# Optimization experiments

Hardware: AMD Instinct MI355X
Metric: run time of the kernel (lower is better)

## Reference

```python
import jax, jax.numpy as jnp
import numpy as np

B, H0, W0, C, NH, WS, SHIFT = 32, 48, 48, 384, 12, 12, 6
N = WS * WS
TAB = 2 * WS - 1  # 23


def _window_partition(x, ws):
    b, h, w, c = x.shape
    x = x.reshape(b, h // ws, ws, w // ws, ws, c)
    return x.transpose(0, 1, 3, 2, 4, 5).reshape(-1, ws, ws, c)


def _window_reverse(win, ws, h, w):
    b = win.shape[0] // (h * w // ws // ws)
    x = win.reshape(b, h // ws, w // ws, ws, ws, -1)
    return x.transpose(0, 1, 3, 2, 4, 5).reshape(b, h, w, -1)


def _ln(y, g, b):
    m = y.mean(-1, keepdims=True)
    v = y.var(-1, keepdims=True)
    return (y - m) * jax.lax.rsqrt(v + 1e-5) * g + b


def setup_inputs() -> dict:
    key = jax.random.key(0)
    ks = jax.random.split(key, 12)
    s = 0.02
    # relative coords table, normalized to [-1, 1]
    rng = np.arange(-(WS - 1), WS, dtype=np.float32) / (WS - 1)
    table = np.stack(np.meshgrid(rng, rng, indexing='ij'), axis=-1)[None]  # (1,23,23,2)
    # relative position index
    ch, cw = np.meshgrid(np.arange(WS), np.arange(WS), indexing='ij')
    coords = np.stack([ch, cw]).reshape(2, -1)
    rel = coords[:, :, None] - coords[:, None, :] + (WS - 1)
    rpi = (rel[0] * TAB + rel[1]).astype(np.int32)  # (N,N)
    # shifted-window attention mask
    img = np.zeros((1, H0, W0, 1), dtype=np.float32)
    cnt = 0
    sl = (slice(0, -WS), slice(-WS, -SHIFT), slice(-SHIFT, None))
    for hs in sl:
        for ws_ in sl:
            img[:, hs, ws_, :] = cnt
            cnt += 1
    mw = img.reshape(1, H0 // WS, WS, W0 // WS, WS, 1).transpose(0, 1, 3, 2, 4, 5).reshape(-1, N)
    diff = mw[:, None, :] - mw[:, :, None]
    attn_mask = np.where(diff != 0, -100.0, 0.0).astype(np.float32)  # (nW,N,N)
    Ch = C * 4
    return {
        'x': jax.random.normal(ks[0], (B, H0 * W0, C), jnp.float32),
        'relative_coords_table': jnp.asarray(table),
        'relative_position_index': jnp.asarray(rpi),
        'attn_mask': jnp.asarray(attn_mask),
        'qkv_w': jax.random.normal(ks[1], (C, 3 * C), jnp.float32) * s,
        'q_bias': jnp.zeros((C,), jnp.float32),
        'v_bias': jnp.zeros((C,), jnp.float32),
        'logit_scale': jnp.log(10.0 * jnp.ones((NH, 1, 1), jnp.float32)),
        'cpb_w1': jax.random.normal(ks[2], (2, 512), jnp.float32) * s,
        'cpb_b1': jnp.zeros((512,), jnp.float32),
        'cpb_w2': jax.random.normal(ks[3], (512, NH), jnp.float32) * s,
        'proj_w': jax.random.normal(ks[4], (C, C), jnp.float32) * s,
        'proj_b': jnp.zeros((C,), jnp.float32),
        'norm1_g': jnp.ones((C,), jnp.float32),
        'norm1_b': jnp.zeros((C,), jnp.float32),
        'norm2_g': jnp.ones((C,), jnp.float32),
        'norm2_b': jnp.zeros((C,), jnp.float32),
        'fc1_w': jax.random.normal(ks[5], (C, Ch), jnp.float32) * s,
        'fc1_b': jnp.zeros((Ch,), jnp.float32),
        'fc2_w': jax.random.normal(ks[6], (Ch, C), jnp.float32) * s,
        'fc2_b': jnp.zeros((C,), jnp.float32),
        'H': H0,
        'W': W0,
    }


def reference(x, relative_coords_table, relative_position_index, attn_mask,
              qkv_w, q_bias, v_bias, logit_scale, cpb_w1, cpb_b1, cpb_w2,
              proj_w, proj_b, norm1_g, norm1_b, norm2_g, norm2_b,
              fc1_w, fc1_b, fc2_w, fc2_b, H, W):
    b, L, c = x.shape
    hd = c // NH
    shortcut = x
    x4 = x.reshape(b, H, W, c)
    shifted = jnp.roll(x4, (-SHIFT, -SHIFT), axis=(1, 2))
    xw = _window_partition(shifted, WS).reshape(-1, N, c)  # (B_, N, C)
    qkv_bias = jnp.concatenate([q_bias, jnp.zeros_like(q_bias), v_bias])
    qkv = xw @ qkv_w + qkv_bias
    qkv = qkv.reshape(-1, N, 3, NH, hd).transpose(2, 0, 3, 1, 4)  # (3,B_,h,N,d)
    q, k, v = qkv[0], qkv[1], qkv[2]
    qn = q / jnp.maximum(jnp.linalg.norm(q, axis=-1, keepdims=True), 1e-12)
    kn = k / jnp.maximum(jnp.linalg.norm(k, axis=-1, keepdims=True), 1e-12)
    attn = jnp.einsum('bhnd,bhmd->bhnm', qn, kn)
    scale = jnp.exp(jnp.minimum(logit_scale, jnp.log(100.0)))  # clamp max=log(1/0.01)
    attn = attn * scale
    tab = jax.nn.relu(relative_coords_table @ cpb_w1 + cpb_b1) @ cpb_w2  # (1,23,23,h)
    tab = tab.reshape(-1, NH)
    bias = tab[relative_position_index.reshape(-1)].reshape(N, N, NH).transpose(2, 0, 1)
    bias = 16.0 * jax.nn.sigmoid(bias)
    attn = attn + bias[None]
    nW = attn_mask.shape[0]
    attn = attn.reshape(b, nW, NH, N, N) + attn_mask[None, :, None]
    attn = jax.nn.softmax(attn.reshape(-1, NH, N, N), axis=-1)
    out = jnp.einsum('bhnm,bhmd->bhnd', attn, v).transpose(0, 2, 1, 3).reshape(-1, N, c)
    out = out @ proj_w + proj_b
    out = _window_reverse(out.reshape(-1, WS, WS, c), WS, H, W)
    x4 = jnp.roll(out, (SHIFT, SHIFT), axis=(1, 2)).reshape(b, H * W, c)
    x = shortcut + _ln(x4, norm1_g, norm1_b)
    h = jax.nn.gelu(x @ fc1_w + fc1_b, approximate=False) @ fc2_w + fc2_b
    x = x + _ln(h, norm2_g, norm2_b)
    return x
```

## Files before the change

kernel.cpp:

```cpp
#include <hip/hip_runtime.h>


typedef unsigned int uint32;
typedef unsigned short u16;
typedef __attribute__((ext_vector_type(4))) float f32x4;
typedef __attribute__((ext_vector_type(8))) __bf16 bf16x8;

static __device__ __forceinline__ u16 f2bf(float f) {
    union { float f; uint32 u; } v; v.f = f;
    uint32 r = v.u + 0x7fffu + ((v.u >> 16) & 1u);
    return (u16)(r >> 16);
}
static __device__ __forceinline__ float bf2f(u16 h) {
    union { uint32 u; float f; } v; v.u = ((uint32)h) << 16; return v.f;
}
static __device__ __forceinline__ uint32 pack2(float a, float b) {
    return (uint32)f2bf(a) | ((uint32)f2bf(b) << 16);
}
static __device__ __forceinline__ float blo(uint32 u){ union{uint32 u;float f;}v; v.u=u<<16; return v.f; }
static __device__ __forceinline__ float bhi(uint32 u){ union{uint32 u;float f;}v; v.u=u&0xffff0000u; return v.f; }

typedef __attribute__((address_space(1))) const void gas_void;
typedef __attribute__((address_space(3))) void las_void;
static __device__ __forceinline__ void glds16(const void* g, void* l) {
    __builtin_amdgcn_global_load_lds((gas_void*)g, (las_void*)l, 16, 0, 0);
}

#define SWZ(c, row) ((c) ^ ((((row) >> 1) & 3) << 3))

#define VMCNT(N) asm volatile("s_waitcnt vmcnt(" #N ")" ::: "memory")
#define BARM() do { asm volatile("" ::: "memory"); __builtin_amdgcn_s_barrier(); asm volatile("" ::: "memory"); } while (0)

static __device__ __forceinline__ float fast_gelu(float x) {
    float z = x * 0.70710678118654752f;
    float az = fabsf(z);
    float t = __builtin_amdgcn_rcpf(fmaf(0.3275911f, az, 1.0f));
    float p = t * (0.254829592f + t * (-0.284496736f + t * (1.421413741f
              + t * (-1.453152027f + t * 1.061405429f))));
    float e = __expf(-z * z);
    float er = copysignf(fmaf(-p, e, 1.0f), z);
    return 0.5f * x * (1.0f + er);
}


__global__ void wt_convert(const float* __restrict__ W, u16* __restrict__ WT, int K, int N) {
    long idx = (long)blockIdx.x * 256 + threadIdx.x;
    long tot = (long)K * N;
    if (idx >= tot) return;
    int n = (int)(idx / K), k = (int)(idx - (long)n * K);
    WT[(long)n * K + SWZ(k, n)] = f2bf(W[(long)k * N + n]);
}

__global__ void build_qkv_bias(const float* __restrict__ qb, const float* __restrict__ vb,
                               float* __restrict__ outb) {
    int c = blockIdx.x * 256 + threadIdx.x;
    if (c >= 1152) return;
    outb[c] = (c < 384) ? qb[c] : ((c < 768) ? 0.f : vb[c - 768]);
}

__global__ void cpb_tab(const float* __restrict__ table, const float* __restrict__ w1,
                        const float* __restrict__ b1, const float* __restrict__ w2,
                        float* __restrict__ tab) {
    __shared__ float hid[512];
    int e = blockIdx.x;
    float tx = table[e * 2 + 0], ty = table[e * 2 + 1];
    for (int u = threadIdx.x; u < 512; u += 256)
        hid[u] = fmaxf(tx * w1[u] + ty * w1[512 + u] + b1[u], 0.f);
    __syncthreads();
    if (threadIdx.x < 12) {
        float s = 0.f;
        for (int u = 0; u < 512; ++u) s += hid[u] * w2[u * 12 + threadIdx.x];
        tab[e * 12 + threadIdx.x] = s;
    }
}

__global__ void cpb_bias(const float* __restrict__ tab, const int* __restrict__ rpi,
                         float* __restrict__ bias16) {
    int idx = blockIdx.x * 256 + threadIdx.x;
    if (idx >= 12 * 144 * 144) return;
    int h = idx / 20736, ij = idx - h * 20736;
    float t = tab[rpi[ij] * 12 + h];
    bias16[idx] = 16.f / (1.f + __expf(-t));
}

__global__ void gather_xbf(const float* __restrict__ x, u16* __restrict__ xw) {
    int idx = blockIdx.x * 256 + threadIdx.x;
    if (idx >= 73728 * 48) return;
    int row = idx / 48, c = (idx - row * 48) * 8;
    int win = row / 144, n = row - win * 144;
    int b = win >> 4, wi = win & 15;
    int r = n / 12, cc = n - r * 12;
    int sh = ((wi >> 2) * 12 + r + 6) % 48;
    int sw = ((wi & 3) * 12 + cc + 6) % 48;
    long src = ((long)(b * 2304 + sh * 48 + sw)) * 384 + c;
    float4 f0 = *(const float4*)(x + src);
    float4 f1 = *(const float4*)(x + src + 4);
    uint4 o;
    o.x = pack2(f0.x, f0.y); o.y = pack2(f0.z, f0.w);
    o.z = pack2(f1.x, f1.y); o.w = pack2(f1.z, f1.w);
    *(uint4*)(xw + (long)row * 384 + SWZ(c, row)) = o;
}


enum { EPI_QKV = 0, EPI_PLAIN = 1, EPI_GELU = 2 };

template<int EPI, bool OSWZ>
__global__ __launch_bounds__(256) void gemm_k(
    const u16* __restrict__ Ag, const u16* __restrict__ Bg,
    const float* __restrict__ bias, u16* __restrict__ outp,
    int N, int K, int ntn)
{
    __shared__ __align__(16) u16 As[3][128 * 32];
    __shared__ __align__(16) u16 Bs[3][128 * 32];
    const int tid = threadIdx.x, lane = tid & 63, wid = tid >> 6;
    const int qq = gridDim.x >> 3;
    const int wg = (blockIdx.x & 7) * qq + (blockIdx.x >> 3);
    const int mIdx = wg / ntn, nIdx = wg - mIdx * ntn;
    const int m0 = mIdx << 7, n0 = nIdx << 7;

    const int wrow = (wid >> 1) << 6, wcol = (wid & 1) << 6;
    const int fr = lane & 15, gsel = lane >> 4;

    const int s_r = (wid << 5) + (lane >> 2);
    const int s_g = (lane & 3) << 3;
    const long a_base = (long)(m0 + s_r) * K + s_g;
    const long b_base = (long)(n0 + s_r) * K + s_g;
    const long qstep = (long)16 * K;

    auto stage = [&](int buf, int kt) {
        const int k0 = kt << 5;
#pragma unroll
        for (int q = 0; q < 2; ++q) {
            glds16(Ag + a_base + qstep * q + k0, &As[buf][(wid * 32 + q * 16) * 32]);
            glds16(Bg + b_base + qstep * q + k0, &Bs[buf][(wid * 32 + q * 16) * 32]);
        }
    };

    int arow[4], acol[4], brow[4], bcol[4];
#pragma unroll
    for (int i = 0; i < 4; ++i) {
        arow[i] = wrow + i * 16 + fr; acol[i] = SWZ(gsel * 8, arow[i]);
        brow[i] = wcol + i * 16 + fr; bcol[i] = SWZ(gsel * 8, brow[i]);
    }

    f32x4 acc[4][4];
    const f32x4 zero4 = {0.f, 0.f, 0.f, 0.f};
#pragma unroll
    for (int i = 0; i < 4; ++i)
#pragma unroll
        for (int j = 0; j < 4; ++j) acc[i][j] = zero4;

    auto compute = [&](int buf) {
        bf16x8 af[4], bg[4];
#pragma unroll
        for (int i = 0; i < 4; ++i) af[i] = *(const bf16x8*)&As[buf][arow[i] * 32 + acol[i]];
#pragma unroll
        for (int j = 0; j < 4; ++j) bg[j] = *(const bf16x8*)&Bs[buf][brow[j] * 32 + bcol[j]];
#pragma unroll
        for (int i = 0; i < 4; ++i)
#pragma unroll
            for (int j = 0; j < 4; ++j)
                acc[i][j] = __builtin_amdgcn_mfma_f32_16x16x32_bf16(af[i], bg[j], acc[i][j], 0, 0, 0);
    };

    const int nk = K >> 5;
    stage(0, 0);
    stage(1, 1);
    int cur = 0, nxt = 2;
    for (int kt = 0; kt < nk - 1; ++kt) {
        VMCNT(4);
        BARM();
        if (kt + 2 < nk) { stage(nxt, kt + 2); nxt = (nxt == 2) ? 0 : nxt + 1; }
        compute(cur);
        cur = (cur == 2) ? 0 : cur + 1;
    }
    VMCNT(0);
    BARM();
    compute(cur);

    const int rbase = gsel << 2;
    if constexpr (EPI == EPI_QKV) {
        long coloff[4];
        float bv[4];
#pragma unroll
        for (int j = 0; j < 4; ++j) {
            int gn0 = n0 + wcol + j * 16;
            int which = gn0 / 384;
            int c = gn0 - which * 384;
            coloff[j] = (long)(which * 12 + (c >> 5)) * 4608 + (c & 31);
            bv[j] = bias[gn0 + fr];
        }
#pragma unroll
        for (int i = 0; i < 4; ++i) {
            long rowoff[4];
#pragma unroll
            for (int r = 0; r < 4; ++r) {
                int gm = m0 + wrow + i * 16 + rbase + r;
                int win = gm / 144, n = gm - win * 144;
                rowoff[r] = (long)win * 165888 + n * 32;
            }
#pragma unroll
            for (int j = 0; j < 4; ++j)
#pragma unroll
                for (int r = 0; r < 4; ++r)
                    outp[rowoff[r] + coloff[j] + fr] = f2bf(acc[i][j][r] + bv[j]);
        }
    } else {
        float bv[4];
#pragma unroll
        for (int j = 0; j < 4; ++j) bv[j] = bias[n0 + wcol + j * 16 + fr];
#pragma unroll
        for (int i = 0; i < 4; ++i) {
#pragma unroll
            for (int r = 0; r < 4; ++r) {
                const int gm = m0 + wrow + i * 16 + rbase + r;
                u16* orow = outp + (long)gm * N;
                const int sx = OSWZ ? (((gm >> 1) & 3) << 3) : 0;
#pragma unroll
                for (int j = 0; j < 4; ++j) {
                    const int gn = n0 + wcol + j * 16 + fr;
                    float v = acc[i][j][r] + bv[j];
                    if constexpr (EPI == EPI_GELU) v = fast_gelu(v);
                    orow[gn ^ sx] = f2bf(v);
                }
            }
        }
    }
}


__global__ __launch_bounds__(192) void attn_k(
    const u16* __restrict__ qkv,
    const float* __restrict__ bias16,
    const float* __restrict__ mask,
    const float* __restrict__ lsc,
    u16* __restrict__ attn_o)
{
    __shared__ __align__(16) u16 KL[144][40];
    __shared__ __align__(16) u16 VT[32][168];
    __shared__ __align__(16) u16 PL[3][16][168];
    const int blk = blockIdx.x;
    const int win = blk / 12, head = blk - win * 12;
    const int tid = threadIdx.x, lane = tid & 63, wid = tid >> 6;
    const long base = ((long)win * 36 + head) * 4608;
    const u16* Qp = qkv + base;
    const u16* Kp = qkv + base + 12 * 4608;
    const u16* Vp = qkv + base + 24 * 4608;
    const float scale = __expf(fminf(lsc[head], 4.6051701859880914f));

    if (tid < 144) {
        const uint4* s = (const uint4*)(Kp + tid * 32);
        uint4 uu[4] = { s[0], s[1], s[2], s[3] };
        float f[32];
#pragma unroll
        for (int q = 0; q < 4; ++q) {
            f[q*8+0]=blo(uu[q].x); f[q*8+1]=bhi(uu[q].x);
            f[q*8+2]=blo(uu[q].y); f[q*8+3]=bhi(uu[q].y);
            f[q*8+4]=blo(uu[q].z); f[q*8+5]=bhi(uu[q].z);
            f[q*8+6]=blo(uu[q].w); f[q*8+7]=bhi(uu[q].w);
        }
        float ss = 0.f;
#pragma unroll
        for (int i = 0; i < 32; ++i) ss += f[i] * f[i];
        float inv = 1.f / fmaxf(sqrtf(ss), 1e-12f);
        uint32 pk[16];
#pragma unroll
        for (int i = 0; i < 16; ++i) pk[i] = pack2(f[2*i] * inv, f[2*i+1] * inv);
        uint4* d = (uint4*)&KL[tid][0];
        d[0] = make_uint4(pk[0], pk[1], pk[2], pk[3]);
        d[1] = make_uint4(pk[4], pk[5], pk[6], pk[7]);
        d[2] = make_uint4(pk[8], pk[9], pk[10], pk[11]);
        d[3] = make_uint4(pk[12], pk[13], pk[14], pk[15]);
        const uint4* sv = (const uint4*)(Vp + tid * 32);
        uint4 vv[4] = { sv[0], sv[1], sv[2], sv[3] };
        u16 vs[32];
#pragma unroll
        for (int q = 0; q < 4; ++q) {
            vs[q*8+0] = (u16)(vv[q].x & 0xffffu); vs[q*8+1] = (u16)(vv[q].x >> 16);
            vs[q*8+2] = (u16)(vv[q].y & 0xffffu); vs[q*8+3] = (u16)(vv[q].y >> 16);
            vs[q*8+4] = (u16)(vv[q].z & 0xffffu); vs[q*8+5] = (u16)(vv[q].z >> 16);
            vs[q*8+6] = (u16)(vv[q].w & 0xffffu); vs[q*8+7] = (u16)(vv[q].w >> 16);
        }
#pragma unroll
        for (int d2 = 0; d2 < 32; ++d2) VT[d2][tid] = vs[d2];
    }
    for (int idx = tid; idx < 512; idx += 192) VT[idx >> 4][144 + (idx & 15)] = 0;
    __syncthreads();

    const int fr = lane & 15, fk = (lane >> 4) << 3, rb = (lane >> 4) << 2;
    const int wim = win & 15;
    const f32x4 zero4 = {0.f, 0.f, 0.f, 0.f};

    for (int s = wid; s < 9; s += 3) {
        const uint4 qu = *(const uint4*)(Qp + (s * 16 + fr) * 32 + fk);
        float qf[8];
        qf[0]=blo(qu.x); qf[1]=bhi(qu.x); qf[2]=blo(qu.y); qf[3]=bhi(qu.y);
        qf[4]=blo(qu.z); qf[5]=bhi(qu.z); qf[6]=blo(qu.w); qf[7]=bhi(qu.w);
        float ss = 0.f;
#pragma unroll
        for (int i = 0; i < 8; ++i) ss += qf[i] * qf[i];
        ss += __shfl_xor(ss, 16);
        ss += __shfl_xor(ss, 32);
        float qinv = scale / fmaxf(sqrtf(ss), 1e-12f);
        union { uint32 u[4]; bf16x8 v; } cv;
#pragma unroll
        for (int i = 0; i < 4; ++i) cv.u[i] = pack2(qf[2*i] * qinv, qf[2*i+1] * qinv);
        bf16x8 aq = cv.v;

        f32x4 sacc[9];
#pragma unroll
        for (int jt = 0; jt < 9; ++jt) sacc[jt] = zero4;
#pragma unroll
        for (int jt = 0; jt < 9; ++jt) {
            bf16x8 bk = *(const bf16x8*)&KL[jt * 16 + fr][fk];
            sacc[jt] = __builtin_amdgcn_mfma_f32_16x16x32_bf16(aq, bk, sacc[jt], 0, 0, 0);
        }
        float mx[4] = {-1e30f, -1e30f, -1e30f, -1e30f};
#pragma unroll
        for (int jt = 0; jt < 9; ++jt) {
            int gj = jt * 16 + fr;
#pragma unroll
            for (int r = 0; r < 4; ++r) {
                int gi = s * 16 + rb + r;
                float v = sacc[jt][r] + bias16[(head * 144 + gi) * 144 + gj]
                                      + mask[(wim * 144 + gi) * 144 + gj];
                sacc[jt][r] = v;
                mx[r] = fmaxf(mx[r], v);
            }
        }
#pragma unroll
        for (int r = 0; r < 4; ++r) {
#pragma unroll
            for (int o = 1; o < 16; o <<= 1) mx[r] = fmaxf(mx[r], __shfl_xor(mx[r], o));
        }
        float sm[4] = {0.f, 0.f, 0.f, 0.f};
#pragma unroll
        for (int jt = 0; jt < 9; ++jt)
#pragma unroll
            for (int r = 0; r < 4; ++r) {
                float e = __expf(sacc[jt][r] - mx[r]);
                sacc[jt][r] = e;
                sm[r] += e;
            }
#pragma unroll
        for (int r = 0; r < 4; ++r) {
#pragma unroll
            for (int o = 1; o < 16; o <<= 1) sm[r] += __shfl_xor(sm[r], o);
            sm[r] = 1.f / sm[r];
        }
#pragma unroll
        for (int jt = 0; jt < 9; ++jt)
#pragma unroll
            for (int r = 0; r < 4; ++r)
                PL[wid][rb + r][jt * 16 + fr] = f2bf(sacc[jt][r]);
#pragma unroll
        for (int r = 0; r < 4; ++r) PL[wid][rb + r][144 + fr] = 0;

        f32x4 oa0 = zero4, oa1 = zero4;
#pragma unroll
        for (int kt = 0; kt < 5; ++kt) {
            bf16x8 ap  = *(const bf16x8*)&PL[wid][fr][kt * 32 + fk];
            bf16x8 bv0 = *(const bf16x8*)&VT[fr][kt * 32 + fk];
            bf16x8 bv1 = *(const bf16x8*)&VT[16 + fr][kt * 32 + fk];
            oa0 = __builtin_amdgcn_mfma_f32_16x16x32_bf16(ap, bv0, oa0, 0, 0, 0);
            oa1 = __builtin_amdgcn_mfma_f32_16x16x32_bf16(ap, bv1, oa1, 0, 0, 0);
        }
#pragma unroll
        for (int r = 0; r < 4; ++r) {
            long row = (long)win * 144 + s * 16 + rb + r;
            int c0 = head * 32 + fr, c1 = head * 32 + 16 + fr;
            attn_o[row * 384 + SWZ(c0, row)] = f2bf(oa0[r] * sm[r]);
            attn_o[row * 384 + SWZ(c1, row)] = f2bf(oa1[r] * sm[r]);
        }
    }
}


__global__ __launch_bounds__(256) void ln1_k(
    const u16* __restrict__ pin, const float* __restrict__ x,
    const float* __restrict__ g, const float* __restrict__ bb,
    u16* __restrict__ y1b)
{
    const int token = blockIdx.x * 4 + (threadIdx.x >> 6);
    const int lane = threadIdx.x & 63;
    int b = token / 2304, hw = token - b * 2304;
    int h = hw / 48, w = hw - h * 48;
    int sh = h + 42; if (sh >= 48) sh -= 48;
    int sw = w + 42; if (sw >= 48) sw -= 48;
    int wh = sh / 12, r = sh - wh * 12;
    int ww = sw / 12, cc = sw - ww * 12;
    long srow = (long)(b * 16 + wh * 4 + ww) * 144 + r * 12 + cc;
    const u16* src = pin + srow * 384;
    float v[6];
    {
        const ushort2* s2 = (const ushort2*)src;
#pragma unroll
        for (int i = 0; i < 3; ++i) {
            ushort2 p = s2[lane * 3 + i];
            v[i * 2] = bf2f(p.x); v[i * 2 + 1] = bf2f(p.y);
        }
    }
    float s1 = 0.f, s2 = 0.f;
#pragma unroll
    for (int i = 0; i < 6; ++i) { s1 += v[i]; s2 += v[i] * v[i]; }
#pragma unroll
    for (int o = 1; o < 64; o <<= 1) { s1 += __shfl_xor(s1, o); s2 += __shfl_xor(s2, o); }
    float mean = s1 * (1.f / 384.f);
    float var = s2 * (1.f / 384.f) - mean * mean;
    float rs = rsqrtf(var + 1e-5f);
    const float* rr = x + (long)token * 384;
    u16* oo = y1b + (long)token * 384;
#pragma unroll
    for (int i = 0; i < 6; ++i) {
        int c = lane * 6 + i;
        oo[SWZ(c, token)] = f2bf(rr[c] + (v[i] - mean) * rs * g[c] + bb[c]);
    }
}

__global__ __launch_bounds__(256) void ln2_k(
    const u16* __restrict__ t2, const u16* __restrict__ y1b,
    const float* __restrict__ g, const float* __restrict__ bb,
    float* __restrict__ outp)
{
    const int token = blockIdx.x * 4 + (threadIdx.x >> 6);
    const int lane = threadIdx.x & 63;
    const u16* src = t2 + (long)token * 384;
    float v[6];
    {
        const ushort2* s2 = (const ushort2*)src;
#pragma unroll
        for (int i = 0; i < 3; ++i) {
            ushort2 p = s2[lane * 3 + i];
            v[i * 2] = bf2f(p.x); v[i * 2 + 1] = bf2f(p.y);
        }
    }
    float s1 = 0.f, s2 = 0.f;
#pragma unroll
    for (int i = 0; i < 6; ++i) { s1 += v[i]; s2 += v[i] * v[i]; }
#pragma unroll
    for (int o = 1; o < 64; o <<= 1) { s1 += __shfl_xor(s1, o); s2 += __shfl_xor(s2, o); }
    float mean = s1 * (1.f / 384.f);
    float var = s2 * (1.f / 384.f) - mean * mean;
    float rs = rsqrtf(var + 1e-5f);
    const u16* rr = y1b + (long)token * 384;
    float* oo = outp + (long)token * 384;
#pragma unroll
    for (int i = 0; i < 6; ++i) {
        int c = lane * 6 + i;
        oo[c] = bf2f(rr[SWZ(c, token)]) + (v[i] - mean) * rs * g[c] + bb[c];
    }
}


extern "C" void kernel_launch(void* const* d_in, const int* in_sizes, int n_in,
                              void* d_out, int out_size, void* d_ws, size_t ws_size,
                              hipStream_t stream) {
    (void)in_sizes; (void)n_in; (void)out_size; (void)ws_size;
    const float* x      = (const float*)d_in[0];
    const float* table  = (const float*)d_in[1];
    const int*   rpi    = (const int*)d_in[2];
    const float* mask   = (const float*)d_in[3];
    const float* qkv_w  = (const float*)d_in[4];
    const float* q_bias = (const float*)d_in[5];
    const float* v_bias = (const float*)d_in[6];
    const float* lsc    = (const float*)d_in[7];
    const float* cpb_w1 = (const float*)d_in[8];
    const float* cpb_b1 = (const float*)d_in[9];
    const float* cpb_w2 = (const float*)d_in[10];
    const float* proj_w = (const float*)d_in[11];
    const float* proj_b = (const float*)d_in[12];
    const float* n1g    = (const float*)d_in[13];
    const float* n1b    = (const float*)d_in[14];
    const float* n2g    = (const float*)d_in[15];
    const float* n2b    = (const float*)d_in[16];
    const float* fc1_w  = (const float*)d_in[17];
    const float* fc1_b  = (const float*)d_in[18];
    const float* fc2_w  = (const float*)d_in[19];
    const float* fc2_b  = (const float*)d_in[20];
    float* outp = (float*)d_out;

    char* ws = (char*)d_ws;
    const size_t offA    = 0;
    const size_t offB    = 226492416;
    const size_t offC    = offB + 56623104;
    const size_t offBias = offC + 56623104;
    const size_t offTab  = offBias + 995328;
    const size_t offQW   = offTab + 25600;
    const size_t offPW   = offQW + 884736;
    const size_t offF1   = offPW + 294912;
    const size_t offF2   = offF1 + 1179648;
    const size_t offQB   = offF2 + 1179648;

    u16*   qkvb    = (u16*)(ws + offA);
    u16*   proj_o  = (u16*)(ws + offA);
    u16*   hbuf    = (u16*)(ws + offA);
    u16*   attn_o  = (u16*)(ws + offB);
    u16*   t2      = (u16*)(ws + offB);
    u16*   xw      = (u16*)(ws + offC);
    u16*   y1b     = (u16*)(ws + offC);
    float* bias16  = (float*)(ws + offBias);
    float* tab     = (float*)(ws + offTab);
    u16*   qkv_wT  = (u16*)(ws + offQW);
    u16*   proj_wT = (u16*)(ws + offPW);
    u16*   fc1_wT  = (u16*)(ws + offF1);
    u16*   fc2_wT  = (u16*)(ws + offF2);
    float* qkvbias = (float*)(ws + offQB);

    wt_convert<<<(384 * 1152 + 255) / 256, 256, 0, stream>>>(qkv_w, qkv_wT, 384, 1152);
    wt_convert<<<(384 * 384 + 255) / 256, 256, 0, stream>>>(proj_w, proj_wT, 384, 384);
    wt_convert<<<(384 * 1536 + 255) / 256, 256, 0, stream>>>(fc1_w, fc1_wT, 384, 1536);
    wt_convert<<<(1536 * 384 + 255) / 256, 256, 0, stream>>>(fc2_w, fc2_wT, 1536, 384);
    build_qkv_bias<<<5, 256, 0, stream>>>(q_bias, v_bias, qkvbias);
    cpb_tab<<<529, 256, 0, stream>>>(table, cpb_w1, cpb_b1, cpb_w2, tab);
    cpb_bias<<<(12 * 144 * 144 + 255) / 256, 256, 0, stream>>>(tab, rpi, bias16);
    gather_xbf<<<(73728 * 48 + 255) / 256, 256, 0, stream>>>(x, xw);

    gemm_k<EPI_QKV, false><<<576 * 9, 256, 0, stream>>>(xw, qkv_wT, qkvbias, qkvb, 1152, 384, 9);

    attn_k<<<6144, 192, 0, stream>>>(qkvb, bias16, mask, lsc, attn_o);

    gemm_k<EPI_PLAIN, false><<<576 * 3, 256, 0, stream>>>(attn_o, proj_wT, proj_b, proj_o, 384, 384, 3);

    ln1_k<<<18432, 256, 0, stream>>>(proj_o, x, n1g, n1b, y1b);

    gemm_k<EPI_GELU, true><<<576 * 12, 256, 0, stream>>>(y1b, fc1_wT, fc1_b, hbuf, 1536, 384, 12);

    gemm_k<EPI_PLAIN, false><<<576 * 3, 256, 0, stream>>>(hbuf, fc2_wT, fc2_b, t2, 384, 1536, 3);

    ln2_k<<<18432, 256, 0, stream>>>(t2, y1b, n2g, n2b, outp);
}
```

Baseline: 789.1 us.

## Enlarge GEMM tiles to 256x128 with compile-time K and unrolled pipeline

The GEMM kernel moves from 128x128 tiles with a 2x2 warp layout to 256x128 tiles. Each of the four waves now computes a 64x128 slab, holding a 4x8 grid of MFMA accumulators. K becomes a template parameter, so the triple-buffered main loop is fully unrolled in groups of three with fixed buffer indices. The shared-memory tiles move to 72 KB of dynamic LDS, and launch_bounds now asks for 2 blocks per CU. The goal is more MFMA work per LDS fragment load and less loop and index overhead, at the cost of higher register pressure, half as many blocks, and a larger LDS footprint that may limit occupancy.

```diff
diff --git a/kernel.cpp b/kernel.cpp
--- a/kernel.cpp
+++ b/kernel.cpp
@@ -104,90 +104,103 @@
 
 enum { EPI_QKV = 0, EPI_PLAIN = 1, EPI_GELU = 2 };
 
-template<int EPI, bool OSWZ>
-__global__ __launch_bounds__(256) void gemm_k(
+template<int EPI, bool OSWZ, int NK>
+__global__ __launch_bounds__(256, 2) void gemm_k(
     const u16* __restrict__ Ag, const u16* __restrict__ Bg,
     const float* __restrict__ bias, u16* __restrict__ outp,
-    int N, int K, int ntn)
+    int N, int ntn)
 {
-    __shared__ __align__(16) u16 As[3][128 * 32];
-    __shared__ __align__(16) u16 Bs[3][128 * 32];
+    constexpr int K = NK * 32;
+    extern __shared__ u16 lds[];
+    u16* As = lds;
+    u16* Bs = lds + 24576;
+
     const int tid = threadIdx.x, lane = tid & 63, wid = tid >> 6;
     const int qq = gridDim.x >> 3;
     const int wg = (blockIdx.x & 7) * qq + (blockIdx.x >> 3);
     const int mIdx = wg / ntn, nIdx = wg - mIdx * ntn;
-    const int m0 = mIdx << 7, n0 = nIdx << 7;
-
-    const int wrow = (wid >> 1) << 6, wcol = (wid & 1) << 6;
+    const int m0 = mIdx << 8, n0 = nIdx << 7;
+
+    const int wrow = wid << 6;
     const int fr = lane & 15, gsel = lane >> 4;
 
-    const int s_r = (wid << 5) + (lane >> 2);
-    const int s_g = (lane & 3) << 3;
-    const long a_base = (long)(m0 + s_r) * K + s_g;
-    const long b_base = (long)(n0 + s_r) * K + s_g;
-    const long qstep = (long)16 * K;
+    const int srow = (wid << 4) + (lane >> 2);
+    const int scol = (lane & 3) << 3;
+    const u16* aP[4];
+    const u16* bP[2];
+#pragma unroll
+    for (int q = 0; q < 4; ++q) aP[q] = Ag + (long)(m0 + (q << 6) + srow) * K + scol;
+#pragma unroll
+    for (int q = 0; q < 2; ++q) bP[q] = Bg + (long)(n0 + (q << 6) + srow) * K + scol;
 
     auto stage = [&](int buf, int kt) {
-        const int k0 = kt << 5;
-#pragma unroll
-        for (int q = 0; q < 2; ++q) {
-            glds16(Ag + a_base + qstep * q + k0, &As[buf][(wid * 32 + q * 16) * 32]);
-            glds16(Bg + b_base + qstep * q + k0, &Bs[buf][(wid * 32 + q * 16) * 32]);
-        }
+#pragma unroll
+        for (int q = 0; q < 4; ++q)
+            glds16(aP[q] + (kt << 5), &As[buf * 8192 + ((q << 6) + (wid << 4)) * 32]);
+#pragma unroll
+        for (int q = 0; q < 2; ++q)
+            glds16(bP[q] + (kt << 5), &Bs[buf * 4096 + ((q << 6) + (wid << 4)) * 32]);
     };
 
-    int arow[4], acol[4], brow[4], bcol[4];
+    int arow[4], acol[4], brow[8], bcol[8];
 #pragma unroll
     for (int i = 0; i < 4; ++i) {
-        arow[i] = wrow + i * 16 + fr; acol[i] = SWZ(gsel * 8, arow[i]);
-        brow[i] = wcol + i * 16 + fr; bcol[i] = SWZ(gsel * 8, brow[i]);
-    }
-
-    f32x4 acc[4][4];
+        arow[i] = wrow + i * 16 + fr;
+        acol[i] = (gsel ^ ((arow[i] >> 1) & 3)) << 3;
+    }
+#pragma unroll
+    for (int j = 0; j < 8; ++j) {
+        brow[j] = j * 16 + fr;
+        bcol[j] = (gsel ^ ((brow[j] >> 1) & 3)) << 3;
+    }
+
+    f32x4 acc[4][8];
     const f32x4 zero4 = {0.f, 0.f, 0.f, 0.f};
 #pragma unroll
     for (int i = 0; i < 4; ++i)
 #pragma unroll
-        for (int j = 0; j < 4; ++j) acc[i][j] = zero4;
+        for (int j = 0; j < 8; ++j) acc[i][j] = zero4;
 
     auto compute = [&](int buf) {
-        bf16x8 af[4], bg[4];
-#pragma unroll
-        for (int i = 0; i < 4; ++i) af[i] = *(const bf16x8*)&As[buf][arow[i] * 32 + acol[i]];
-#pragma unroll
-        for (int j = 0; j < 4; ++j) bg[j] = *(const bf16x8*)&Bs[buf][brow[j] * 32 + bcol[j]];
+        const u16* pa = As + buf * 8192;
+        const u16* pb = Bs + buf * 4096;
+        bf16x8 af[4], bg[8];
+#pragma unroll
+        for (int i = 0; i < 4; ++i) af[i] = *(const bf16x8*)&pa[arow[i] * 32 + acol[i]];
+#pragma unroll
+        for (int j = 0; j < 8; ++j) bg[j] = *(const bf16x8*)&pb[brow[j] * 32 + bcol[j]];
 #pragma unroll
         for (int i = 0; i < 4; ++i)
 #pragma unroll
-            for (int j = 0; j < 4; ++j)
+            for (int j = 0; j < 8; ++j)
                 acc[i][j] = __builtin_amdgcn_mfma_f32_16x16x32_bf16(af[i], bg[j], acc[i][j], 0, 0, 0);
     };
 
-    const int nk = K >> 5;
     stage(0, 0);
     stage(1, 1);
-    int cur = 0, nxt = 2;
-    for (int kt = 0; kt < nk - 1; ++kt) {
-        VMCNT(4);
-        BARM();
-        if (kt + 2 < nk) { stage(nxt, kt + 2); nxt = (nxt == 2) ? 0 : nxt + 1; }
-        compute(cur);
-        cur = (cur == 2) ? 0 : cur + 1;
-    }
-    VMCNT(0);
-    BARM();
-    compute(cur);
+#define GITER(KT, BC, BN_) \
+    VMCNT(6); BARM(); stage(BN_, (KT) + 2); compute(BC);
+    for (int g = 0; g < (NK - 1) / 3; ++g) {
+        const int kb = g * 3;
+        GITER(kb + 0, 0, 2);
+        GITER(kb + 1, 1, 0);
+        GITER(kb + 2, 2, 1);
+    }
+#undef GITER
+    VMCNT(6); BARM(); stage(2, NK - 1); compute(0);
+    VMCNT(6); BARM(); compute(1);
+    VMCNT(0); BARM(); compute(2);
 
     const int rbase = gsel << 2;
     if constexpr (EPI == EPI_QKV) {
-        long coloff[4];
-        float bv[4];
-#pragma unroll
-        for (int j = 0; j < 4; ++j) {
-            int gn0 = n0 + wcol + j * 16;
+        long coloff[8];
+        float bv[8];
+#pragma unroll
+        for (int j = 0; j < 8; ++j) {
+            int gn0 = n0 + j * 16;
             int which = gn0 / 384;
             int c = gn0 - which * 384;
-            coloff[j] = (long)(which * 12 + (c >> 5)) * 4608 + (c & 31);
+            coloff[j] = (long)(which * 12 + (c >> 5)) * 4608 + (c & 31) + fr;
             bv[j] = bias[gn0 + fr];
         }
 #pragma unroll
@@ -200,15 +213,15 @@
                 rowoff[r] = (long)win * 165888 + n * 32;
             }
 #pragma unroll
-            for (int j = 0; j < 4; ++j)
+            for (int j = 0; j < 8; ++j)
 #pragma unroll
                 for (int r = 0; r < 4; ++r)
-                    outp[rowoff[r] + coloff[j] + fr] = f2bf(acc[i][j][r] + bv[j]);
+                    outp[rowoff[r] + coloff[j]] = f2bf(acc[i][j][r] + bv[j]);
         }
     } else {
-        float bv[4];
-#pragma unroll
-        for (int j = 0; j < 4; ++j) bv[j] = bias[n0 + wcol + j * 16 + fr];
+        float bv[8];
+#pragma unroll
+        for (int j = 0; j < 8; ++j) bv[j] = bias[n0 + j * 16 + fr];
 #pragma unroll
         for (int i = 0; i < 4; ++i) {
 #pragma unroll
@@ -217,8 +230,8 @@
                 u16* orow = outp + (long)gm * N;
                 const int sx = OSWZ ? (((gm >> 1) & 3) << 3) : 0;
 #pragma unroll
-                for (int j = 0; j < 4; ++j) {
-                    const int gn = n0 + wcol + j * 16 + fr;
+                for (int j = 0; j < 8; ++j) {
+                    const int gn = n0 + j * 16 + fr;
                     float v = acc[i][j][r] + bv[j];
                     if constexpr (EPI == EPI_GELU) v = fast_gelu(v);
                     orow[gn ^ sx] = f2bf(v);
@@ -506,6 +519,15 @@
     u16*   fc2_wT  = (u16*)(ws + offF2);
     float* qkvbias = (float*)(ws + offQB);
 
+    hipFuncSetAttribute((const void*)&gemm_k<EPI_QKV, false, 12>,
+                        hipFuncAttributeMaxDynamicSharedMemorySize, 73728);
+    hipFuncSetAttribute((const void*)&gemm_k<EPI_PLAIN, false, 12>,
+                        hipFuncAttributeMaxDynamicSharedMemorySize, 73728);
+    hipFuncSetAttribute((const void*)&gemm_k<EPI_GELU, true, 12>,
+                        hipFuncAttributeMaxDynamicSharedMemorySize, 73728);
+    hipFuncSetAttribute((const void*)&gemm_k<EPI_PLAIN, false, 48>,
+                        hipFuncAttributeMaxDynamicSharedMemorySize, 73728);
+
     wt_convert<<<(384 * 1152 + 255) / 256, 256, 0, stream>>>(qkv_w, qkv_wT, 384, 1152);
     wt_convert<<<(384 * 384 + 255) / 256, 256, 0, stream>>>(proj_w, proj_wT, 384, 384);
     wt_convert<<<(384 * 1536 + 255) / 256, 256, 0, stream>>>(fc1_w, fc1_wT, 384, 1536);
@@ -515,17 +537,17 @@
     cpb_bias<<<(12 * 144 * 144 + 255) / 256, 256, 0, stream>>>(tab, rpi, bias16);
     gather_xbf<<<(73728 * 48 + 255) / 256, 256, 0, stream>>>(x, xw);
 
-    gemm_k<EPI_QKV, false><<<576 * 9, 256, 0, stream>>>(xw, qkv_wT, qkvbias, qkvb, 1152, 384, 9);
+    gemm_k<EPI_QKV, false, 12><<<288 * 9, 256, 73728, stream>>>(xw, qkv_wT, qkvbias, qkvb, 1152, 9);
 
     attn_k<<<6144, 192, 0, stream>>>(qkvb, bias16, mask, lsc, attn_o);
 
-    gemm_k<EPI_PLAIN, false><<<576 * 3, 256, 0, stream>>>(attn_o, proj_wT, proj_b, proj_o, 384, 384, 3);
+    gemm_k<EPI_PLAIN, false, 12><<<288 * 3, 256, 73728, stream>>>(attn_o, proj_wT, proj_b, proj_o, 384, 3);
 
     ln1_k<<<18432, 256, 0, stream>>>(proj_o, x, n1g, n1b, y1b);
 
-    gemm_k<EPI_GELU, true><<<576 * 12, 256, 0, stream>>>(y1b, fc1_wT, fc1_b, hbuf, 1536, 384, 12);
-
-    gemm_k<EPI_PLAIN, false><<<576 * 3, 256, 0, stream>>>(hbuf, fc2_wT, fc2_b, t2, 384, 1536, 3);
+    gemm_k<EPI_GELU, true, 12><<<288 * 12, 256, 73728, stream>>>(y1b, fc1_wT, fc1_b, hbuf, 1536, 12);
+
+    gemm_k<EPI_PLAIN, false, 48><<<288 * 3, 256, 73728, stream>>>(hbuf, fc2_wT, fc2_b, t2, 384, 3);
 
     ln2_k<<<18432, 256, 0, stream>>>(t2, y1b, n2g, n2b, outp);
 }
```

New measurement: 737.4 us. 6.5% less time.
